# Optimization experiments

Measured on AMD Instinct MI355X. Metric: run time of the kernel, lower is better.

## Reference

```python
import jax, jax.numpy as jnp
import numpy as np

D = H = W = 128
C = 16
VOXEL_SIZE = 0.05  # origin = 0, grid spans [0, 6.4]^3 in world coords
N_POINTS = 2_000_000


def setup_inputs() -> dict:
    key = jax.random.key(0)
    k1, k2 = jax.random.split(key)
    # world-space query points uniformly inside the grid bounds
    points = jax.random.uniform(k1, (N_POINTS, 3), dtype=jnp.float32) * (D * VOXEL_SIZE)
    values = jax.random.normal(k2, (D, H, W, C), dtype=jnp.float32)
    return {"points": points, "values": values}


def reference(points, values):
    # world -> grid coords (origin = 0)
    gc = points / VOXEL_SIZE  # [N, 3]
    x, y, z = gc[:, 0], gc[:, 1], gc[:, 2]

    x0 = jnp.clip(jnp.floor(x).astype(jnp.int32), 0, D - 1)
    y0 = jnp.clip(jnp.floor(y).astype(jnp.int32), 0, H - 1)
    z0 = jnp.clip(jnp.floor(z).astype(jnp.int32), 0, W - 1)
    x1 = jnp.clip(x0 + 1, 0, D - 1)
    y1 = jnp.clip(y0 + 1, 0, H - 1)
    z1 = jnp.clip(z0 + 1, 0, W - 1)

    # fractional offsets (computed against the clipped floor index, as in source)
    xd = (x - x0.astype(x.dtype))[:, None]
    yd = (y - y0.astype(y.dtype))[:, None]
    zd = (z - z0.astype(z.dtype))[:, None]

    # flatten grid for efficient single-axis gather
    flat = values.reshape(D * H * W, C)

    def gather(xi, yi, zi):
        lin = (xi * H + yi) * W + zi  # [N]
        return jnp.take(flat, lin, axis=0)  # [N, C]

    c000 = gather(x0, y0, z0)
    c001 = gather(x0, y0, z1)
    c010 = gather(x0, y1, z0)
    c011 = gather(x0, y1, z1)
    c100 = gather(x1, y0, z0)
    c101 = gather(x1, y0, z1)
    c110 = gather(x1, y1, z0)
    c111 = gather(x1, y1, z1)

    c00 = c000 * (1 - xd) + c100 * xd
    c01 = c001 * (1 - xd) + c101 * xd
    c10 = c010 * (1 - xd) + c110 * xd
    c11 = c011 * (1 - xd) + c111 * xd
    c0 = c00 * (1 - yd) + c10 * yd
    c1 = c01 * (1 - yd) + c11 * yd
    return c0 * (1 - zd) + c1 * zd  # [N, C]
```

## Files before the change

### kernel.cpp

```cpp
#include <hip/hip_runtime.h>


#define DD 128
#define HH 128
#define WW 128
#define NBX 16
#define NB (NBX * NBX * NBX)
#define CAP 640
#define CUR_STRIDE 16

typedef float fvec4 __attribute__((ext_vector_type(4)));

__device__ __forceinline__ float4 lerp4(float4 a, float4 b, float t) {
    return make_float4(fmaf(b.x - a.x, t, a.x),
                       fmaf(b.y - a.y, t, a.y),
                       fmaf(b.z - a.z, t, a.z),
                       fmaf(b.w - a.w, t, a.w));
}

__device__ __forceinline__ int clampi(int v, int lo, int hi) {
    return min(max(v, lo), hi);
}

__device__ __forceinline__ float4 trilerp_point(const float4* __restrict__ values,
                                                float x, float y, float z, int c4) {
    float fx = floorf(x), fy = floorf(y), fz = floorf(z);
    int x0 = clampi((int)fx, 0, DD - 1);
    int y0 = clampi((int)fy, 0, HH - 1);
    int z0 = clampi((int)fz, 0, WW - 1);
    int x1 = min(x0 + 1, DD - 1);
    int y1 = min(y0 + 1, HH - 1);
    int z1 = min(z0 + 1, WW - 1);

    float xd = x - (float)x0;
    float yd = y - (float)y0;
    float zd = z - (float)z0;

    #define VIDX(xi, yi, zi) ((((((xi) << 7) + (yi)) << 7) + (zi)) * 4 + c4)
    float4 c000 = values[VIDX(x0, y0, z0)];
    float4 c001 = values[VIDX(x0, y0, z1)];
    float4 c010 = values[VIDX(x0, y1, z0)];
    float4 c011 = values[VIDX(x0, y1, z1)];
    float4 c100 = values[VIDX(x1, y0, z0)];
    float4 c101 = values[VIDX(x1, y0, z1)];
    float4 c110 = values[VIDX(x1, y1, z0)];
    float4 c111 = values[VIDX(x1, y1, z1)];
    #undef VIDX

    float4 c00 = lerp4(c000, c100, xd);
    float4 c01 = lerp4(c001, c101, xd);
    float4 c10 = lerp4(c010, c110, xd);
    float4 c11 = lerp4(c011, c111, xd);
    float4 c0  = lerp4(c00, c10, yd);
    float4 c1  = lerp4(c01, c11, yd);
    return lerp4(c0, c1, zd);
}

__global__ __launch_bounds__(256) void scatter_kernel(
    const float* __restrict__ points,
    unsigned* __restrict__ cursors,
    float4* __restrict__ recs,
    const float4* __restrict__ values,
    float4* __restrict__ out,
    int n_points)
{
    int p = blockIdx.x * blockDim.x + threadIdx.x;
    if (p >= n_points) return;

    float x = points[p * 3 + 0] * 20.0f;
    float y = points[p * 3 + 1] * 20.0f;
    float z = points[p * 3 + 2] * 20.0f;

    int bx = clampi((int)floorf(x), 0, DD - 1) >> 3;
    int by = clampi((int)floorf(y), 0, HH - 1) >> 3;
    int bz = clampi((int)floorf(z), 0, WW - 1) >> 3;
    int b = (bx * NBX + by) * NBX + bz;

    unsigned pos = atomicAdd(&cursors[b * CUR_STRIDE], 1u);
    if (pos < CAP) {
        float4 r = make_float4(x, y, z, __uint_as_float((unsigned)p));
        recs[(unsigned)b * CAP + pos] = r;
    } else {
        #pragma unroll
        for (int c = 0; c < 4; ++c)
            out[p * 4 + c] = trilerp_point(values, x, y, z, c);
    }
}

__global__ __launch_bounds__(256) void interp_kernel(
    const float4* __restrict__ recs,
    const unsigned* __restrict__ cursors,
    const float4* __restrict__ values,
    float4* __restrict__ out)
{
    int b = blockIdx.x;
    unsigned cnt = cursors[b * CUR_STRIDE];
    if (cnt > CAP) cnt = CAP;
    unsigned base = (unsigned)b * CAP;
    int c4 = threadIdx.x & 3;

    for (unsigned j = threadIdx.x >> 2; j < cnt; j += 64) {
        float4 r = recs[base + j];
        float4 res = trilerp_point(values, r.x, r.y, r.z, c4);
        unsigned idx = __float_as_uint(r.w);
        __builtin_nontemporal_store(*(fvec4*)&res, (fvec4*)(out + ((size_t)idx * 4 + c4)));
    }
}

__global__ __launch_bounds__(256) void trilerp_kernel(
    const float* __restrict__ points,
    const float4* __restrict__ values,
    float4* __restrict__ out,
    int n_points)
{
    int t = blockIdx.x * blockDim.x + threadIdx.x;
    int p = t >> 2;
    int c4 = t & 3;
    if (p >= n_points) return;

    float x = points[p * 3 + 0] * 20.0f;
    float y = points[p * 3 + 1] * 20.0f;
    float z = points[p * 3 + 2] * 20.0f;
    out[t] = trilerp_point(values, x, y, z, c4);
}

extern "C" void kernel_launch(void* const* d_in, const int* in_sizes, int n_in,
                              void* d_out, int out_size, void* d_ws, size_t ws_size,
                              hipStream_t stream) {
    const float* points = (const float*)d_in[0];
    const float4* values = (const float4*)d_in[1];
    float4* out = (float4*)d_out;

    int n_points = in_sizes[0] / 3;

    const size_t cursors_bytes = (size_t)NB * CUR_STRIDE * sizeof(unsigned);
    const size_t recs_bytes = (size_t)NB * CAP * sizeof(float4);
    const size_t required = cursors_bytes + recs_bytes;

    if (d_ws != nullptr && ws_size >= required) {
        unsigned* cursors = (unsigned*)d_ws;
        float4* recs = (float4*)((char*)d_ws + cursors_bytes);

        hipMemsetAsync(cursors, 0, cursors_bytes, stream);

        int blocks = (n_points + 255) / 256;
        scatter_kernel<<<blocks, 256, 0, stream>>>(points, cursors, recs, values, out, n_points);
        interp_kernel<<<NB, 256, 0, stream>>>(recs, cursors, values, out);
    } else {
        int total_threads = n_points * 4;
        int blocks = (total_threads + 255) / 256;
        trilerp_kernel<<<blocks, 256, 0, stream>>>(points, values, out, n_points);
    }
}
```

Baseline: 480.1 us.

## Stage per-brick voxel halo in LDS and split bins into atomic partitions

The interp kernel now loads a 9x9x9x16 halo of the value grid for its 8^3 brick into shared memory and does the eight corner gathers from LDS rather than global memory. Bins are split into four partitions keyed on block index, which spreads atomic contention on the cursors. Record writes become nontemporal stores. The cost is about 47KB of LDS per block, which limits occupancy, plus more fallback points if a partition overflows its smaller capacity of 152.

```diff
diff --git a/kernel.cpp b/kernel.cpp
--- a/kernel.cpp
+++ b/kernel.cpp
@@ -6,7 +6,8 @@
 #define WW 128
 #define NBX 16
 #define NB (NBX * NBX * NBX)
-#define CAP 640
+#define NPART 4
+#define CAP2 152
 #define CUR_STRIDE 16
 
 typedef float fvec4 __attribute__((ext_vector_type(4)));
@@ -66,6 +67,7 @@
 {
     int p = blockIdx.x * blockDim.x + threadIdx.x;
     if (p >= n_points) return;
+    int part = blockIdx.x & (NPART - 1);
 
     float x = points[p * 3 + 0] * 20.0f;
     float y = points[p * 3 + 1] * 20.0f;
@@ -74,12 +76,12 @@
     int bx = clampi((int)floorf(x), 0, DD - 1) >> 3;
     int by = clampi((int)floorf(y), 0, HH - 1) >> 3;
     int bz = clampi((int)floorf(z), 0, WW - 1) >> 3;
-    int b = (bx * NBX + by) * NBX + bz;
-
-    unsigned pos = atomicAdd(&cursors[b * CUR_STRIDE], 1u);
-    if (pos < CAP) {
-        float4 r = make_float4(x, y, z, __uint_as_float((unsigned)p));
-        recs[(unsigned)b * CAP + pos] = r;
+    int sb = (part * NB) + ((bx * NBX + by) * NBX + bz);
+
+    unsigned pos = atomicAdd(&cursors[sb * CUR_STRIDE], 1u);
+    if (pos < CAP2) {
+        fvec4 r = { x, y, z, __uint_as_float((unsigned)p) };
+        __builtin_nontemporal_store(r, (fvec4*)(recs + (size_t)sb * CAP2 + pos));
     } else {
         #pragma unroll
         for (int c = 0; c < 4; ++c)
@@ -93,18 +95,69 @@
     const float4* __restrict__ values,
     float4* __restrict__ out)
 {
+    __shared__ float4 sv[9 * 9 * 9 * 4];
+
     int b = blockIdx.x;
-    unsigned cnt = cursors[b * CUR_STRIDE];
-    if (cnt > CAP) cnt = CAP;
-    unsigned base = (unsigned)b * CAP;
+    int bz = b & 15, by = (b >> 4) & 15, bx = b >> 8;
+    int X0 = bx << 3, Y0 = by << 3, Z0 = bz << 3;
+
+    for (int e = threadIdx.x; e < 9 * 9 * 9 * 4; e += 256) {
+        int v = e >> 2, c = e & 3;
+        int i = v / 81;
+        int r = v - i * 81;
+        int j = r / 9;
+        int k = r - j * 9;
+        int gx = min(X0 + i, DD - 1);
+        int gy = min(Y0 + j, HH - 1);
+        int gz = min(Z0 + k, WW - 1);
+        sv[e] = values[((((gx << 7) + gy) << 7) + gz) * 4 + c];
+    }
+    __syncthreads();
+
     int c4 = threadIdx.x & 3;
 
-    for (unsigned j = threadIdx.x >> 2; j < cnt; j += 64) {
-        float4 r = recs[base + j];
-        float4 res = trilerp_point(values, r.x, r.y, r.z, c4);
-        unsigned idx = __float_as_uint(r.w);
-        __builtin_nontemporal_store(*(fvec4*)&res, (fvec4*)(out + ((size_t)idx * 4 + c4)));
-    }
+    #define SIDX(i, j, k) (((((i) * 9) + (j)) * 9 + (k)) * 4 + c4)
+    for (int part = 0; part < NPART; ++part) {
+        int sb = part * NB + b;
+        unsigned cnt = cursors[sb * CUR_STRIDE];
+        if (cnt > CAP2) cnt = CAP2;
+        const float4* rp = recs + (size_t)sb * CAP2;
+
+        for (unsigned j = threadIdx.x >> 2; j < cnt; j += 64) {
+            float4 r = rp[j];
+            float x = r.x, y = r.y, z = r.z;
+
+            float fx = floorf(x), fy = floorf(y), fz = floorf(z);
+            int x0 = clampi((int)fx, 0, DD - 1);
+            int y0 = clampi((int)fy, 0, HH - 1);
+            int z0 = clampi((int)fz, 0, WW - 1);
+            float xd = x - (float)x0;
+            float yd = y - (float)y0;
+            float zd = z - (float)z0;
+
+            int xl = x0 - X0, yl = y0 - Y0, zl = z0 - Z0;
+            float4 c000 = sv[SIDX(xl,     yl,     zl    )];
+            float4 c001 = sv[SIDX(xl,     yl,     zl + 1)];
+            float4 c010 = sv[SIDX(xl,     yl + 1, zl    )];
+            float4 c011 = sv[SIDX(xl,     yl + 1, zl + 1)];
+            float4 c100 = sv[SIDX(xl + 1, yl,     zl    )];
+            float4 c101 = sv[SIDX(xl + 1, yl,     zl + 1)];
+            float4 c110 = sv[SIDX(xl + 1, yl + 1, zl    )];
+            float4 c111 = sv[SIDX(xl + 1, yl + 1, zl + 1)];
+
+            float4 c00 = lerp4(c000, c100, xd);
+            float4 c01 = lerp4(c001, c101, xd);
+            float4 c10 = lerp4(c010, c110, xd);
+            float4 c11 = lerp4(c011, c111, xd);
+            float4 c0  = lerp4(c00, c10, yd);
+            float4 c1  = lerp4(c01, c11, yd);
+            float4 res = lerp4(c0, c1, zd);
+
+            unsigned idx = __float_as_uint(r.w);
+            __builtin_nontemporal_store(*(fvec4*)&res, (fvec4*)(out + ((size_t)idx * 4 + c4)));
+        }
+    }
+    #undef SIDX
 }
 
 __global__ __launch_bounds__(256) void trilerp_kernel(
@@ -133,8 +186,8 @@
 
     int n_points = in_sizes[0] / 3;
 
-    const size_t cursors_bytes = (size_t)NB * CUR_STRIDE * sizeof(unsigned);
-    const size_t recs_bytes = (size_t)NB * CAP * sizeof(float4);
+    const size_t cursors_bytes = (size_t)NPART * NB * CUR_STRIDE * sizeof(unsigned);
+    const size_t recs_bytes = (size_t)NPART * NB * CAP2 * sizeof(float4);
     const size_t required = cursors_bytes + recs_bytes;
 
     if (d_ws != nullptr && ws_size >= required) {
```

Result: faster. 439.7 us (-8.4%).
